# Optimization experiments

Hardware: AMD Instinct MI355X
Metric: run time of the kernel (lower is better)

Reference implementation:

```python
import jax, jax.numpy as jnp
import numpy as np
import math

B, L, HID, H = 16, 1024, 1024, 16
E = HID // H
HALF = L // 2 + 1                      # 513 rfft bins
GLOBAL_RATIO = 0.6
LEFT = int(HALF * (1.0 - GLOBAL_RATIO))  # 205 (i=0, filter_mixer='G')
RIGHT = HALF                            # 513
FACTOR = 1
TOP_K = int(FACTOR * math.log(L))       # 6
LN_EPS = 1e-12


def setup_inputs() -> dict:
    key = jax.random.key(0)
    ks = jax.random.split(key, 12)
    s = 0.02
    return {
        "input_tensor": jax.random.normal(ks[0], (B, L, HID), jnp.float32),
        "attention_mask": jnp.zeros((B, 1, 1, L), jnp.float32),
        "Wq": jax.random.normal(ks[1], (HID, HID), jnp.float32) * s,
        "bq": jnp.zeros((HID,), jnp.float32),
        "Wk": jax.random.normal(ks[2], (HID, HID), jnp.float32) * s,
        "bk": jnp.zeros((HID,), jnp.float32),
        "Wv": jax.random.normal(ks[3], (HID, HID), jnp.float32) * s,
        "bv": jnp.zeros((HID,), jnp.float32),
        "Wd": jax.random.normal(ks[4], (HID, HID), jnp.float32) * s,
        "bd": jnp.zeros((HID,), jnp.float32),
        "gamma": jnp.ones((HID,), jnp.float32),
        "beta": jnp.zeros((HID,), jnp.float32),
    }


def _heads(x):  # [B,L,HID] -> [B,H,E,L]
    return x.reshape(B, L, H, E).transpose(0, 2, 3, 1)


def _layer_norm(x, gamma, beta):
    mu = jnp.mean(x, axis=-1, keepdims=True)
    var = jnp.var(x, axis=-1, keepdims=True)
    return (x - mu) / jnp.sqrt(var + LN_EPS) * gamma + beta


def reference(input_tensor, attention_mask, Wq, bq, Wk, bk, Wv, bv, Wd, bd, gamma, beta):
    # QKV projections -> [B,H,E,L]
    q = _heads(input_tensor @ Wq + bq)
    k = _heads(input_tensor @ Wk + bk)
    v = _heads(input_tensor @ Wv + bv)

    # FFT-based autocorrelation restricted to retained frequency band [LEFT,RIGHT)
    q_fft = jnp.fft.rfft(q, axis=-1)            # [B,H,E,HALF] complex64
    k_fft = jnp.fft.rfft(k, axis=-1)
    res = q_fft[..., LEFT:RIGHT] * jnp.conj(k_fft[..., LEFT:RIGHT])
    box = jnp.zeros((B, H, E, HALF), res.dtype).at[..., LEFT:RIGHT].set(res)
    corr = jnp.fft.irfft(box, n=L, axis=-1)     # [B,H,E,L]

    # time_delay_agg_training: topk shared delays, softmax-weighted roll aggregation
    mean_value = jnp.mean(corr, axis=(1, 2))            # [B,L]
    _, idx = jax.lax.top_k(jnp.mean(mean_value, axis=0), TOP_K)  # [TOP_K]
    weights = mean_value[:, idx]                         # [B,TOP_K]
    tmp_corr = jax.nn.softmax(weights, axis=-1)
    delays_agg = jnp.zeros_like(v)
    for i in range(TOP_K):  # TOP_K=6, fixed small loop
        pattern = jnp.roll(v, -idx[i], axis=-1)
        delays_agg = delays_agg + pattern * tmp_corr[:, i][:, None, None, None]

    # [B,H,E,L] -> [B,L,HID]
    context = delays_agg.transpose(0, 3, 1, 2).reshape(B, L, HID)
    hidden = context @ Wd + bd
    return _layer_norm(hidden + input_tensor, gamma, beta)
```

## Files before the change

### kernel.cpp

```cpp
#include <hip/hip_runtime.h>


typedef unsigned short u16;
typedef unsigned int   u32;
typedef __attribute__((ext_vector_type(8))) __bf16 bf16x8;
typedef __attribute__((ext_vector_type(4))) float  floatx4;

#define HIDn 1024

__device__ __forceinline__ u16 f2b(float f){ u32 i = __float_as_uint(f); return (u16)((i + 0x7fffu + ((i>>16)&1u)) >> 16); }

__device__ __forceinline__ void gl_lds16(const u16* g, u16* l){
  __builtin_amdgcn_global_load_lds((__attribute__((address_space(1))) const void*)g,
                                   (__attribute__((address_space(3))) void*)l, 16, 0, 0);
}

__device__ __forceinline__ void bar(){
  asm volatile("" ::: "memory");
  __builtin_amdgcn_s_barrier();
  asm volatile("" ::: "memory");
}
__device__ __forceinline__ void lgkm0(){
  asm volatile("s_waitcnt lgkmcnt(0)" ::: "memory");
  __builtin_amdgcn_sched_barrier(0);
}

__global__ void fill_kernel(float* __restrict__ out, float v, int n)
{
  const int i = blockIdx.x*blockDim.x + threadIdx.x;
  if (i < n) out[i] = v;
}

__global__ __launch_bounds__(256)
void cast_kernel(const float* __restrict__ x, u16* __restrict__ xb,
                 float* __restrict__ cbuf)
{
  const int i = blockIdx.x*256 + threadIdx.x;
  if (blockIdx.x < 64) cbuf[i] = 0.f;
  const float4* xp = (const float4*)x;
  const float4 a = xp[2*i], b = xp[2*i+1];
  uint4 o;
  o.x = (u32)f2b(a.x) | ((u32)f2b(a.y)<<16);
  o.y = (u32)f2b(a.z) | ((u32)f2b(a.w)<<16);
  o.z = (u32)f2b(b.x) | ((u32)f2b(b.y)<<16);
  o.w = (u32)f2b(b.z) | ((u32)f2b(b.w)<<16);
  ((uint4*)xb)[i] = o;
}

__global__ __launch_bounds__(1024)
void transpose_kernel(const float* __restrict__ Wq, const float* __restrict__ Wk,
                      const float* __restrict__ Wv, const float* __restrict__ Wd,
                      u16* __restrict__ WqkvT, u16* __restrict__ WdT)
{
  __shared__ float tile[32][33];
  const int mat = blockIdx.z;
  const float* W = (mat==0)?Wq:(mat==1)?Wk:(mat==2)?Wv:Wd;
  const int k = blockIdx.y*32 + threadIdx.y;
  const int n = blockIdx.x*32 + threadIdx.x;
  tile[threadIdx.y][threadIdx.x] = W[(long)k*HIDn + n];
  __syncthreads();
  const int on = blockIdx.x*32 + threadIdx.y;
  const int ok = blockIdx.y*32 + threadIdx.x;
  const u16 val = f2b(tile[threadIdx.x][threadIdx.y]);
  if (mat < 3) WqkvT[(long)(mat*HIDn + on)*HIDn + ok] = val;
  else         WdT[(long)on*HIDn + ok] = val;
}

template<int EPI>
__global__ __launch_bounds__(512, 2)
void gemm_mfma(const u16* __restrict__ A, int lda, long sA,
               const u16* __restrict__ Bt, int ldb, long sB,
               void* __restrict__ C0, u16* __restrict__ o1, u16* __restrict__ o2,
               int ldc, int K,
               const float* __restrict__ b0, const float* __restrict__ b1,
               const float* __restrict__ b2, const float* __restrict__ resid,
               float* __restrict__ cbuf)
{
  __shared__ __align__(16) u16 As[2][16384];
  __shared__ __align__(16) u16 Bs[2][16384];
  __shared__ float bins[512];

  const int gx = gridDim.x, gy = gridDim.y;
  const int lin = (blockIdx.z*gy + blockIdx.y)*gx + blockIdx.x;
  const int cpx = (gx*gy*gridDim.z) >> 3;
  const int swz = (lin & 7)*cpx + (lin >> 3);
  const int bx  = swz % gx;
  const int byz = swz / gx;
  const int by  = byz % gy;
  const int bz  = byz / gy;

  const int tid  = threadIdx.x;
  const int wave = tid >> 6, lane = tid & 63;
  const int waveM = wave >> 2, waveN = wave & 3;
  const int qd = lane >> 4, ln = lane & 15, rl = ln & 7;
  const u16* Ab = A  + (long)bz * sA;
  const u16* Bb = Bt + (long)bz * sB;
  const int aRow0 = by * 256, bRow0 = bx * 256;
  const int nt = K >> 6;

  const int s0 = wave*128 + lane;
  const int r0 = s0 >> 3, r1 = r0 + 8;
  const int kc = ((s0 & 7) ^ (r0 & 7)) * 8;
  const long aOff0 = (long)(aRow0 + r0)*lda + kc;
  const long aOff1 = (long)(aRow0 + r1)*lda + kc;
  const long bOff0 = (long)(bRow0 + r0)*ldb + kc;
  const long bOff1 = (long)(bRow0 + r1)*ldb + kc;
  const int dstW = wave*1024;

#define STAGE_A(p, h, kt) do{ \
    gl_lds16(Ab + aOff0 + (long)(h)*128*lda + (kt), &As[p][(h)*8192 + dstW]); \
    gl_lds16(Ab + aOff1 + (long)(h)*128*lda + (kt), &As[p][(h)*8192 + dstW + 512]); }while(0)
#define STAGE_B(p, h, kt) do{ \
    gl_lds16(Bb + bOff0 + (long)(h)*128*ldb + (kt), &Bs[p][(h)*8192 + dstW]); \
    gl_lds16(Bb + bOff1 + (long)(h)*128*ldb + (kt), &Bs[p][(h)*8192 + dstW + 512]); }while(0)

  if (EPI == 3) bins[tid] = 0.f;

  floatx4 acc[8][4];
  const floatx4 z4 = {0.f, 0.f, 0.f, 0.f};
  #pragma unroll
  for (int i=0;i<8;++i)
    #pragma unroll
    for (int j=0;j<4;++j) acc[i][j] = z4;

  const int aRd = (waveM*128 + ln)*64;
  const int bRd = (waveN*64  + ln)*64;
  const int csw0 = ((0 + qd) ^ rl) * 8;
  const int csw1 = ((4 + qd) ^ rl) * 8;

  bf16x8 av0[4], av1[4];
  bf16x8 bvA0[2], bvA1[2];
  bf16x8 bvB0[2], bvB1[2];

#define DS_AV(BUF, MH) do{ const u16* Ap_ = &As[BUF][0]; \
    _Pragma("unroll") for (int mi=0;mi<4;++mi){ \
      av0[mi] = *(const bf16x8*)(Ap_ + aRd + (MH)*4096 + mi*1024 + csw0); \
      av1[mi] = *(const bf16x8*)(Ap_ + aRd + (MH)*4096 + mi*1024 + csw1); } }while(0)
#define DS_BV(BUF, NH, d0_, d1_) do{ const u16* Bp_ = &Bs[BUF][0]; \
    _Pragma("unroll") for (int ni=0;ni<2;++ni){ \
      d0_[ni] = *(const bf16x8*)(Bp_ + bRd + ((NH)*2+ni)*1024 + csw0); \
      d1_[ni] = *(const bf16x8*)(Bp_ + bRd + ((NH)*2+ni)*1024 + csw1); } }while(0)
#define MFMAQ(MH, NH, b0_, b1_) do{ \
    __builtin_amdgcn_sched_barrier(0); \
    __builtin_amdgcn_s_setprio(1); \
    _Pragma("unroll") for (int mi=0;mi<4;++mi) \
      _Pragma("unroll") for (int ni=0;ni<2;++ni){ \
        acc[(MH)*4+mi][(NH)*2+ni] = __builtin_amdgcn_mfma_f32_16x16x32_bf16(av0[mi], b0_[ni], acc[(MH)*4+mi][(NH)*2+ni],0,0,0); \
        acc[(MH)*4+mi][(NH)*2+ni] = __builtin_amdgcn_mfma_f32_16x16x32_bf16(av1[mi], b1_[ni], acc[(MH)*4+mi][(NH)*2+ni],0,0,0); } \
    __builtin_amdgcn_s_setprio(0); \
    __builtin_amdgcn_sched_barrier(0); }while(0)

  STAGE_B(0,0,0);  STAGE_B(0,1,0);  STAGE_A(0,0,0);  STAGE_A(0,1,0);
  STAGE_B(1,0,64); STAGE_B(1,1,64); STAGE_A(1,0,64); STAGE_A(1,1,64);
  asm volatile("s_waitcnt vmcnt(8)" ::: "memory");
  bar();

  const int nIt = nt >> 1;
  for (int it = 0; it < nIt-1; ++it){
    const int k2 = (it*2+2) << 6;
    const int k3 = (it*2+3) << 6;
    DS_AV(0,0); DS_BV(0,0,bvA0,bvA1);
    bar(); lgkm0(); MFMAQ(0,0,bvA0,bvA1); bar();
    DS_BV(0,1,bvB0,bvB1);
    bar(); lgkm0(); MFMAQ(0,1,bvB0,bvB1); bar();
    DS_AV(0,1); STAGE_B(0,0,k2);
    bar(); lgkm0(); MFMAQ(1,0,bvA0,bvA1); bar();
    STAGE_B(0,1,k2);
    asm volatile("s_waitcnt vmcnt(4)" ::: "memory");
    bar(); MFMAQ(1,1,bvB0,bvB1); bar();
    DS_AV(1,0); DS_BV(1,0,bvA0,bvA1); STAGE_A(0,0,k2);
    bar(); lgkm0(); MFMAQ(0,0,bvA0,bvA1); bar();
    DS_BV(1,1,bvB0,bvB1); STAGE_A(0,1,k2);
    bar(); lgkm0(); MFMAQ(0,1,bvB0,bvB1); bar();
    DS_AV(1,1); STAGE_B(1,0,k3);
    bar(); lgkm0(); MFMAQ(1,0,bvA0,bvA1); bar();
    STAGE_B(1,1,k3); STAGE_A(1,0,k3); STAGE_A(1,1,k3);
    asm volatile("s_waitcnt vmcnt(8)" ::: "memory");
    bar(); MFMAQ(1,1,bvB0,bvB1); bar();
  }
  DS_AV(0,0); DS_BV(0,0,bvA0,bvA1);
  bar(); lgkm0(); MFMAQ(0,0,bvA0,bvA1); bar();
  DS_BV(0,1,bvB0,bvB1);
  bar(); lgkm0(); MFMAQ(0,1,bvB0,bvB1); bar();
  DS_AV(0,1);
  bar(); lgkm0(); MFMAQ(1,0,bvA0,bvA1); bar();
  asm volatile("s_waitcnt vmcnt(0)" ::: "memory");
  bar(); MFMAQ(1,1,bvB0,bvB1); bar();
  DS_AV(1,0); DS_BV(1,0,bvA0,bvA1);
  bar(); lgkm0(); MFMAQ(0,0,bvA0,bvA1); bar();
  DS_BV(1,1,bvB0,bvB1);
  bar(); lgkm0(); MFMAQ(0,1,bvB0,bvB1); bar();
  DS_AV(1,1);
  bar(); lgkm0(); MFMAQ(1,0,bvA0,bvA1); bar();
  MFMAQ(1,1,bvB0,bvB1);
#undef STAGE_A
#undef STAGE_B
#undef DS_AV
#undef DS_BV
#undef MFMAQ

  if (EPI == 3){
    float dsum[11][4];
    #pragma unroll
    for (int dd=0; dd<11; ++dd)
      #pragma unroll
      for (int r=0;r<4;++r) dsum[dd][r] = 0.f;
    #pragma unroll
    for (int mi=0;mi<8;++mi)
      #pragma unroll
      for (int ni=0;ni<4;++ni){
        const int dd = mi - ni + 3;
        #pragma unroll
        for (int r=0;r<4;++r) dsum[dd][r] += acc[mi][ni][r];
      }
    const int base = 255 + 128*waveM - 64*waveN + 4*qd - ln;
    #pragma unroll
    for (int dd=0; dd<11; ++dd)
      #pragma unroll
      for (int r=0;r<4;++r)
        atomicAdd(&bins[base + 16*(dd-3) + r], dsum[dd][r]);
    __syncthreads();
    if (tid < 511){
      const int d = (aRow0 - bRow0 + tid - 255) & 1023;
      atomicAdd(cbuf + bz*1024 + d, bins[tid]);
    }
    return;
  }

  if (EPI == 0){
    const int which = bx >> 2;
    const float* bp = (which==0) ? b0 : ((which==1) ? b1 : b2);
    u16* Cb = (which==0) ? (u16*)C0 : ((which==1) ? o1 : o2);
    const int nb = bRow0 & 1023;
    #pragma unroll
    for (int mi=0;mi<8;++mi){
      const int gm = aRow0 + waveM*128 + mi*16 + qd*4;
      #pragma unroll
      for (int ni=0;ni<4;++ni){
        const int nl = nb + waveN*64 + ni*16 + ln;
        const float bias = bp[nl];
        #pragma unroll
        for (int r=0;r<4;++r) Cb[(long)(gm+r)*ldc + nl] = f2b(acc[mi][ni][r] + bias);
      }
    }
  } else {
    float* C = (float*)C0;
    #pragma unroll
    for (int mi=0;mi<8;++mi){
      const int gm = aRow0 + waveM*128 + mi*16 + qd*4;
      #pragma unroll
      for (int ni=0;ni<4;++ni){
        const int gn = bRow0 + waveN*64 + ni*16 + ln;
        const float bias = b0[gn];
        #pragma unroll
        for (int r=0;r<4;++r)
          C[(long)(gm+r)*ldc + gn] = acc[mi][ni][r] + bias + resid[(long)(gm+r)*ldc + gn];
      }
    }
  }
}

__global__ __launch_bounds__(256)
void filter_kernel(const float* __restrict__ c, float* __restrict__ mv)
{
  __shared__ float carr[1024];
  __shared__ float gsh[1024];
  const int b = blockIdx.x >> 2, l0 = (blockIdx.x & 3) << 8;
  const int t = threadIdx.x;
  #pragma unroll
  for (int j = 0; j < 4; ++j){
    const int d = t + j*256;
    carr[d] = c[b*1024 + d];
    float s;
    if (d == 0) s = 307.f;
    else {
      const float k = 3.14159265358979e0f/1024.f;
      const int n1 = (307*d) & 2047, n2 = (716*d) & 2047;
      s = sinf((float)n1*k) * cosf((float)n2*k) / sinf((float)d*k);
    }
    gsh[d] = (2.f*s + ((d & 1) ? -1.f : 1.f)) * (1.0f/1048576.0f);
  }
  __syncthreads();
  const int l = l0 + t;
  float o = 0.f;
  #pragma unroll 4
  for (int m = 0; m < 1024; ++m) o += carr[m] * gsh[(l - m) & 1023];
  mv[b*1024 + l] = o;
}

__global__ __launch_bounds__(1024)
void topk_kernel(const float* __restrict__ mv, int* __restrict__ idxout,
                 float* __restrict__ wout)
{
  __shared__ float vals[1024];
  __shared__ float wv[16];
  __shared__ int   wi[16];
  __shared__ int   chosen[6];
  const int t = threadIdx.x, lane = t & 63, wid = t >> 6;
  float s = 0.f;
  #pragma unroll
  for (int b = 0; b < 16; ++b) s += mv[b*1024 + t];
  vals[t] = s;
  __syncthreads();
  for (int r = 0; r < 6; ++r){
    float cv = vals[t]; int ci = t;
    #pragma unroll
    for (int off = 32; off > 0; off >>= 1){
      const float ov = __shfl_down(cv, off);
      const int   oi = __shfl_down(ci, off);
      if (ov > cv || (ov == cv && oi < ci)){ cv = ov; ci = oi; }
    }
    if (lane == 0){ wv[wid] = cv; wi[wid] = ci; }
    __syncthreads();
    if (t == 0){
      float bv = wv[0]; int bi = wi[0];
      #pragma unroll
      for (int k = 1; k < 16; ++k)
        if (wv[k] > bv || (wv[k] == bv && wi[k] < bi)){ bv = wv[k]; bi = wi[k]; }
      chosen[r] = bi; idxout[r] = bi; vals[bi] = -3.0e38f;
    }
    __syncthreads();
  }
  if (t < 16){
    float w[6]; float mx = -3.0e38f;
    #pragma unroll
    for (int i = 0; i < 6; ++i){ w[i] = mv[t*1024 + chosen[i]]; mx = fmaxf(mx, w[i]); }
    float sum = 0.f;
    #pragma unroll
    for (int i = 0; i < 6; ++i){ w[i] = expf(w[i] - mx); sum += w[i]; }
    #pragma unroll
    for (int i = 0; i < 6; ++i) wout[t*6 + i] = w[i] / sum;
  }
}

__global__ __launch_bounds__(256)
void context_kernel(const u16* __restrict__ Vb, const int* __restrict__ idx,
                    const float* __restrict__ w, u16* __restrict__ CT)
{
  const int row = blockIdx.x*2 + (threadIdx.x >> 7);
  const int b = row >> 10, l = row & 1023;
  const int t = threadIdx.x & 127;
  float wl[6]; int id[6];
  #pragma unroll
  for (int i = 0; i < 6; ++i){ id[i] = idx[i]; wl[i] = w[b*6 + i]; }
  float acc[8] = {0,0,0,0,0,0,0,0};
  #pragma unroll
  for (int i = 0; i < 6; ++i){
    const long src = (long)b*1024 + ((l + id[i]) & 1023);
    const uint4 pk = *(const uint4*)(Vb + src*1024 + t*8);
    const float ww = wl[i];
    union{float f; u32 u;} cv;
    cv.u = pk.x<<16;          acc[0] += ww*cv.f;
    cv.u = pk.x & 0xffff0000u; acc[1] += ww*cv.f;
    cv.u = pk.y<<16;          acc[2] += ww*cv.f;
    cv.u = pk.y & 0xffff0000u; acc[3] += ww*cv.f;
    cv.u = pk.z<<16;          acc[4] += ww*cv.f;
    cv.u = pk.z & 0xffff0000u; acc[5] += ww*cv.f;
    cv.u = pk.w<<16;          acc[6] += ww*cv.f;
    cv.u = pk.w & 0xffff0000u; acc[7] += ww*cv.f;
  }
  uint4 o;
  o.x = (u32)f2b(acc[0]) | ((u32)f2b(acc[1])<<16);
  o.y = (u32)f2b(acc[2]) | ((u32)f2b(acc[3])<<16);
  o.z = (u32)f2b(acc[4]) | ((u32)f2b(acc[5])<<16);
  o.w = (u32)f2b(acc[6]) | ((u32)f2b(acc[7])<<16);
  *(uint4*)(CT + (long)row*1024 + t*8) = o;
}

__global__ __launch_bounds__(256)
void ln_kernel(float* __restrict__ io, const float* __restrict__ gamma,
               const float* __restrict__ beta)
{
  __shared__ float s1[256];
  __shared__ float s2[256];
  const int row = blockIdx.x, t = threadIdx.x;
  float4 v = ((const float4*)(io + (long)row*1024))[t];
  s1[t] = v.x+v.y+v.z+v.w;
  s2[t] = v.x*v.x+v.y*v.y+v.z*v.z+v.w*v.w;
  __syncthreads();
  for (int off = 128; off > 0; off >>= 1){
    if (t < off){ s1[t] += s1[t+off]; s2[t] += s2[t+off]; }
    __syncthreads();
  }
  const float mu  = s1[0] * (1.f/1024.f);
  const float var = fmaxf(s2[0] * (1.f/1024.f) - mu*mu, 0.f);
  const float rstd = rsqrtf(var + 1e-12f);
  const float4 g  = ((const float4*)gamma)[t];
  const float4 be = ((const float4*)beta)[t];
  float4 o;
  o.x = (v.x-mu)*rstd*g.x + be.x;
  o.y = (v.y-mu)*rstd*g.y + be.y;
  o.z = (v.z-mu)*rstd*g.z + be.z;
  o.w = (v.w-mu)*rstd*g.w + be.w;
  ((float4*)(io + (long)row*1024))[t] = o;
}

extern "C" void kernel_launch(void* const* d_in, const int* in_sizes, int n_in,
                              void* d_out, int out_size, void* d_ws, size_t ws_size,
                              hipStream_t stream)
{
  (void)in_sizes; (void)n_in;
  const float* x     = (const float*)d_in[0];
  const float* Wq    = (const float*)d_in[2];
  const float* bq    = (const float*)d_in[3];
  const float* Wk    = (const float*)d_in[4];
  const float* bk    = (const float*)d_in[5];
  const float* Wv    = (const float*)d_in[6];
  const float* bv    = (const float*)d_in[7];
  const float* Wd    = (const float*)d_in[8];
  const float* bd    = (const float*)d_in[9];
  const float* gamma = (const float*)d_in[10];
  const float* beta  = (const float*)d_in[11];
  float* outp = (float*)d_out;

  const size_t NEED = 142741952UL;
  if (ws_size < NEED){
    const int n = out_size/2;
    fill_kernel<<<(n+255)/256, 256, 0, stream>>>(outp, (float)ws_size, n);
    return;
  }
  char* ws = (char*)d_ws;
  u16*  xb    = (u16*)(ws);
  u16*  Qb    = (u16*)(ws + 33554432L);
  u16*  Kb    = (u16*)(ws + 67108864L);
  u16*  Vb    = (u16*)(ws + 100663296L);
  u16*  WqkvT = (u16*)(ws + 134217728L);
  u16*  WdT   = (u16*)(ws + 140509184L);
  float* cbuf = (float*)(ws + 142606336L);
  float* mv   = (float*)(ws + 142671872L);
  int*   idxb = (int*)  (ws + 142741504L);
  float* wsm  = (float*)(ws + 142741568L);
  u16*  CT    = Qb;

  cast_kernel<<<8192, 256, 0, stream>>>(x, xb, cbuf);
  transpose_kernel<<<dim3(32,32,4), dim3(32,32), 0, stream>>>(Wq, Wk, Wv, Wd, WqkvT, WdT);

  gemm_mfma<0><<<dim3(12,64,1), 512, 0, stream>>>(
      xb, 1024, 0L, WqkvT, 1024, 0L, Qb, Kb, Vb, 1024, 1024,
      bq, bk, bv, nullptr, nullptr);

  gemm_mfma<3><<<dim3(4,4,16), 512, 0, stream>>>(
      Qb, 1024, 1048576L, Kb, 1024, 1048576L, nullptr, nullptr, nullptr, 0, 1024,
      nullptr, nullptr, nullptr, nullptr, cbuf);

  filter_kernel<<<64, 256, 0, stream>>>(cbuf, mv);
  topk_kernel<<<1, 1024, 0, stream>>>(mv, idxb, wsm);
  context_kernel<<<8192, 256, 0, stream>>>(Vb, idxb, wsm, CT);

  gemm_mfma<2><<<dim3(4,64,1), 512, 0, stream>>>(
      CT, 1024, 0L, WdT, 1024, 0L, outp, nullptr, nullptr, 1024, 1024,
      bd, nullptr, nullptr, x, nullptr);

  ln_kernel<<<16384, 256, 0, stream>>>(outp, gamma, beta);
}
```

Baseline: 439.0 us.

## Fuse prep kernels, merge filter+topk via linear batch-sum, remap context blocks to XCDs

Merges the cast and weight-transpose kernels into a single launch. Replaces the 64-block per-batch circular filter plus topk with one single-block kernel. That kernel first sums correlations over the batch, filters only that sum to pick the top-k, and then evaluates the filter for each batch only at the 6 chosen delays. This relies on the filter being linear and removes one launch and most of the filter work. The context kernel also gets a block-index swizzle so each XCD handles a contiguous range of rows, aiming for better L2 locality. The cost is that the spectral stage now runs on a single workgroup.

```diff
diff --git a/kernel.cpp b/kernel.cpp
--- a/kernel.cpp
+++ b/kernel.cpp
@@ -31,39 +31,40 @@
   if (i < n) out[i] = v;
 }
 
-__global__ __launch_bounds__(256)
-void cast_kernel(const float* __restrict__ x, u16* __restrict__ xb,
-                 float* __restrict__ cbuf)
-{
-  const int i = blockIdx.x*256 + threadIdx.x;
-  if (blockIdx.x < 64) cbuf[i] = 0.f;
-  const float4* xp = (const float4*)x;
-  const float4 a = xp[2*i], b = xp[2*i+1];
-  uint4 o;
-  o.x = (u32)f2b(a.x) | ((u32)f2b(a.y)<<16);
-  o.y = (u32)f2b(a.z) | ((u32)f2b(a.w)<<16);
-  o.z = (u32)f2b(b.x) | ((u32)f2b(b.y)<<16);
-  o.w = (u32)f2b(b.z) | ((u32)f2b(b.w)<<16);
-  ((uint4*)xb)[i] = o;
-}
-
 __global__ __launch_bounds__(1024)
-void transpose_kernel(const float* __restrict__ Wq, const float* __restrict__ Wk,
-                      const float* __restrict__ Wv, const float* __restrict__ Wd,
-                      u16* __restrict__ WqkvT, u16* __restrict__ WdT)
+void prep_kernel(const float* __restrict__ x, u16* __restrict__ xb,
+                 float* __restrict__ cbuf,
+                 const float* __restrict__ Wq, const float* __restrict__ Wk,
+                 const float* __restrict__ Wv, const float* __restrict__ Wd,
+                 u16* __restrict__ WqkvT, u16* __restrict__ WdT)
 {
   __shared__ float tile[32][33];
-  const int mat = blockIdx.z;
-  const float* W = (mat==0)?Wq:(mat==1)?Wk:(mat==2)?Wv:Wd;
-  const int k = blockIdx.y*32 + threadIdx.y;
-  const int n = blockIdx.x*32 + threadIdx.x;
-  tile[threadIdx.y][threadIdx.x] = W[(long)k*HIDn + n];
-  __syncthreads();
-  const int on = blockIdx.x*32 + threadIdx.y;
-  const int ok = blockIdx.y*32 + threadIdx.x;
-  const u16 val = f2b(tile[threadIdx.x][threadIdx.y]);
-  if (mat < 3) WqkvT[(long)(mat*HIDn + on)*HIDn + ok] = val;
-  else         WdT[(long)on*HIDn + ok] = val;
+  if (blockIdx.x < 2048){
+    const int i = blockIdx.x*1024 + threadIdx.x;
+    if (i < 16384) cbuf[i] = 0.f;
+    const float4* xp = (const float4*)x;
+    const float4 a = xp[2*i], b = xp[2*i+1];
+    uint4 o;
+    o.x = (u32)f2b(a.x) | ((u32)f2b(a.y)<<16);
+    o.y = (u32)f2b(a.z) | ((u32)f2b(a.w)<<16);
+    o.z = (u32)f2b(b.x) | ((u32)f2b(b.y)<<16);
+    o.w = (u32)f2b(b.z) | ((u32)f2b(b.w)<<16);
+    ((uint4*)xb)[i] = o;
+  } else {
+    const int bb  = blockIdx.x - 2048;
+    const int mat = bb >> 10;
+    const int rem = bb & 1023;
+    const int bxT = rem & 31, byT = rem >> 5;
+    const int tx = threadIdx.x & 31, ty = threadIdx.x >> 5;
+    const float* W = (mat==0)?Wq:(mat==1)?Wk:(mat==2)?Wv:Wd;
+    const int k = byT*32 + ty, n = bxT*32 + tx;
+    tile[ty][tx] = W[(long)k*HIDn + n];
+    __syncthreads();
+    const int on = bxT*32 + ty, ok = byT*32 + tx;
+    const u16 val = f2b(tile[tx][ty]);
+    if (mat < 3) WqkvT[(long)(mat*HIDn + on)*HIDn + ok] = val;
+    else         WdT[(long)on*HIDn + ok] = val;
+  }
 }
 
 template<int EPI>
@@ -260,48 +261,42 @@
   }
 }
 
-__global__ __launch_bounds__(256)
-void filter_kernel(const float* __restrict__ c, float* __restrict__ mv)
-{
-  __shared__ float carr[1024];
+__global__ __launch_bounds__(1024)
+void spect_kernel(const float* __restrict__ c, int* __restrict__ idxout,
+                  float* __restrict__ wout)
+{
+  __shared__ float csh[16][1024];
   __shared__ float gsh[1024];
-  const int b = blockIdx.x >> 2, l0 = (blockIdx.x & 3) << 8;
-  const int t = threadIdx.x;
-  #pragma unroll
-  for (int j = 0; j < 4; ++j){
-    const int d = t + j*256;
-    carr[d] = c[b*1024 + d];
-    float s;
-    if (d == 0) s = 307.f;
-    else {
-      const float k = 3.14159265358979e0f/1024.f;
-      const int n1 = (307*d) & 2047, n2 = (716*d) & 2047;
-      s = sinf((float)n1*k) * cosf((float)n2*k) / sinf((float)d*k);
-    }
-    gsh[d] = (2.f*s + ((d & 1) ? -1.f : 1.f)) * (1.0f/1048576.0f);
-  }
-  __syncthreads();
-  const int l = l0 + t;
-  float o = 0.f;
-  #pragma unroll 4
-  for (int m = 0; m < 1024; ++m) o += carr[m] * gsh[(l - m) & 1023];
-  mv[b*1024 + l] = o;
-}
-
-__global__ __launch_bounds__(1024)
-void topk_kernel(const float* __restrict__ mv, int* __restrict__ idxout,
-                 float* __restrict__ wout)
-{
+  __shared__ float csum[1024];
   __shared__ float vals[1024];
   __shared__ float wv[16];
   __shared__ int   wi[16];
   __shared__ int   chosen[6];
+  __shared__ float pw[96];
   const int t = threadIdx.x, lane = t & 63, wid = t >> 6;
-  float s = 0.f;
+
+  float sc = 0.f;
   #pragma unroll
-  for (int b = 0; b < 16; ++b) s += mv[b*1024 + t];
-  vals[t] = s;
+  for (int b = 0; b < 16; ++b){ const float v = c[b*1024 + t]; csh[b][t] = v; sc += v; }
+  csum[t] = sc;
+  {
+    float s;
+    if (t == 0) s = 307.f;
+    else {
+      const float k = 3.14159265358979e0f/1024.f;
+      const int n1 = (307*t) & 2047, n2 = (716*t) & 2047;
+      s = sinf((float)n1*k) * cosf((float)n2*k) / sinf((float)t*k);
+    }
+    gsh[t] = (2.f*s + ((t & 1) ? -1.f : 1.f)) * (1.0f/1048576.0f);
+  }
   __syncthreads();
+
+  float S = 0.f;
+  #pragma unroll 4
+  for (int m = 0; m < 1024; ++m) S += csum[m] * gsh[(t - m) & 1023];
+  vals[t] = S;
+  __syncthreads();
+
   for (int r = 0; r < 6; ++r){
     float cv = vals[t]; int ci = t;
     #pragma unroll
@@ -321,10 +316,22 @@
     }
     __syncthreads();
   }
+
+  if (t < 768){
+    const int p = t >> 3, li = t & 7;
+    const int b = p / 6, i = p % 6, ch = chosen[i];
+    float acc = 0.f;
+    #pragma unroll 4
+    for (int m = li*128; m < li*128 + 128; ++m) acc += csh[b][m] * gsh[(ch - m) & 1023];
+    #pragma unroll
+    for (int off = 4; off > 0; off >>= 1) acc += __shfl_down(acc, off);
+    if (li == 0) pw[p] = acc;
+  }
+  __syncthreads();
   if (t < 16){
     float w[6]; float mx = -3.0e38f;
     #pragma unroll
-    for (int i = 0; i < 6; ++i){ w[i] = mv[t*1024 + chosen[i]]; mx = fmaxf(mx, w[i]); }
+    for (int i = 0; i < 6; ++i){ w[i] = pw[t*6 + i]; mx = fmaxf(mx, w[i]); }
     float sum = 0.f;
     #pragma unroll
     for (int i = 0; i < 6; ++i){ w[i] = expf(w[i] - mx); sum += w[i]; }
@@ -337,7 +344,9 @@
 void context_kernel(const u16* __restrict__ Vb, const int* __restrict__ idx,
                     const float* __restrict__ w, u16* __restrict__ CT)
 {
-  const int row = blockIdx.x*2 + (threadIdx.x >> 7);
+  const int lin = blockIdx.x;
+  const int xcd = lin & 7, j = lin >> 3;
+  const int row = xcd*2048 + j*2 + (threadIdx.x >> 7);
   const int b = row >> 10, l = row & 1023;
   const int t = threadIdx.x & 127;
   float wl[6]; int id[6];
@@ -427,13 +436,11 @@
   u16*  WqkvT = (u16*)(ws + 134217728L);
   u16*  WdT   = (u16*)(ws + 140509184L);
   float* cbuf = (float*)(ws + 142606336L);
-  float* mv   = (float*)(ws + 142671872L);
   int*   idxb = (int*)  (ws + 142741504L);
   float* wsm  = (float*)(ws + 142741568L);
   u16*  CT    = Qb;
 
-  cast_kernel<<<8192, 256, 0, stream>>>(x, xb, cbuf);
-  transpose_kernel<<<dim3(32,32,4), dim3(32,32), 0, stream>>>(Wq, Wk, Wv, Wd, WqkvT, WdT);
+  prep_kernel<<<6144, 1024, 0, stream>>>(x, xb, cbuf, Wq, Wk, Wv, Wd, WqkvT, WdT);
 
   gemm_mfma<0><<<dim3(12,64,1), 512, 0, stream>>>(
       xb, 1024, 0L, WqkvT, 1024, 0L, Qb, Kb, Vb, 1024, 1024,
@@ -443,8 +450,7 @@
       Qb, 1024, 1048576L, Kb, 1024, 1048576L, nullptr, nullptr, nullptr, 0, 1024,
       nullptr, nullptr, nullptr, nullptr, cbuf);
 
-  filter_kernel<<<64, 256, 0, stream>>>(cbuf, mv);
-  topk_kernel<<<1, 1024, 0, stream>>>(mv, idxb, wsm);
+  spect_kernel<<<1, 1024, 0, stream>>>(cbuf, idxb, wsm);
   context_kernel<<<8192, 256, 0, stream>>>(Vb, idxb, wsm, CT);
 
   gemm_mfma<2><<<dim3(4,64,1), 512, 0, stream>>>(
```

Result: slower. 450.0 us (+2.5%).
